# Performance work log

Measured on AMD Instinct MI355X. Metric: run time of the kernel, lower is better.

## Reference

```python
import jax, jax.numpy as jnp
import numpy as np

DIM = 1024
S_SIZE = 512
M_SIZE = 4096
L_SIZE = 8192
MERGE_THRESHOLD = 0.98
L_ALPHA = 0.1
K_PROMOTE = max(1, S_SIZE // 4)  # torch: min(len(candidates), max(1, s_size//4)); candidates >> s_size here


def _l2norm(x, axis=-1):
    # F.normalize(p=2) with eps clamp
    return x / jnp.maximum(jnp.linalg.norm(x, axis=axis, keepdims=True), 1e-12)


def _update(processed_tokens, s_memory, m_memory, l_memory, m_utility, l_utility, wq, bq, wk, bk, s_ptr):
    cand = processed_tokens.reshape(-1, DIM)
    # --- S tier: scatter top-k-norm candidates into ring buffer (vectorized; K<=S so slots distinct) ---
    norms = jnp.linalg.norm(cand, axis=1)
    _, top_idx = jax.lax.top_k(norms, K_PROMOTE)
    pos = (s_ptr + jnp.arange(K_PROMOTE)) % S_SIZE
    s_mem = s_memory.at[pos].set(cand[top_idx])
    s_ptr_new = (s_ptr + K_PROMOTE) % S_SIZE
    # --- promotion attention (1 head, only attn weights used): pick best short-term slot ---
    q = l_memory.mean(axis=0) @ wq.T + bq                      # [dim]
    kproj = s_mem @ wk.T + bk                                  # [S, dim]
    attn = jax.nn.softmax(kproj @ q / jnp.sqrt(jnp.asarray(DIM, cand.dtype)))
    best_s_idx = jnp.argmax(attn)
    candidate = s_mem[best_s_idx]                              # [dim]

    # --- M tier: promote / merge / replace ---
    def not_full(mm, mu):
        ridx = jnp.argmin(mu)
        return mm.at[ridx].set(candidate), mu.at[ridx].set(mu.mean() + 1e-5)

    def full(mm, mu):
        mm_norm = _l2norm(mm)
        sims = mm_norm @ _l2norm(candidate)                    # [M]
        msi = jnp.argmax(sims)
        sim_cand = sims[msi]

        def merge_with_candidate(mm, mu):
            merged = _l2norm((mm[msi] + candidate) / 2.0)
            return mm.at[msi].set(merged), mu.at[msi].set((mu[msi] + mu.mean()) / 2.0)

        def try_internal_merge(mm, mu):
            # most redundant pair: strict lower triangle of cosine sim matrix
            sim_mat = mm_norm @ mm_norm.T                      # [M, M]
            sim_mat = jnp.where(jnp.triu(jnp.ones((M_SIZE, M_SIZE), bool)), -1.0, sim_mat)
            flat = jnp.argmax(sim_mat)
            internal_sim = sim_mat.reshape(-1)[flat]
            idx1, idx2 = flat // M_SIZE, flat % M_SIZE

            def do_pair_merge(mm, mu):
                merged = _l2norm((mm[idx1] + mm[idx2]) / 2.0)
                mm2 = mm.at[idx1].set(merged).at[idx2].set(candidate)
                mu1 = mu.at[idx1].set((mu[idx1] + mu[idx2]) / 2.0)
                mu2 = mu1.at[idx2].set(mu1.mean() + 1e-5)      # torch recomputes mean after idx1 write
                return mm2, mu2

            def replace_weakest(mm, mu):
                li = jnp.argmin(mu)
                stronger = jnp.linalg.norm(candidate) > jnp.linalg.norm(mm[li])
                mm2 = jnp.where(stronger, mm.at[li].set(candidate), mm)
                mu2 = jnp.where(stronger, mu.at[li].set(mu.mean() + 1e-5), mu)
                return mm2, mu2

            return jax.lax.cond(internal_sim > MERGE_THRESHOLD, do_pair_merge, replace_weakest, mm, mu)

        return jax.lax.cond(sim_cand > MERGE_THRESHOLD, merge_with_candidate, try_internal_merge, mm, mu)

    is_m_full = ~jnp.any(m_utility == 0)
    m_mem, m_util = jax.lax.cond(is_m_full, full, not_full, m_memory, m_utility)
    # --- L tier: consolidate most-used M slot into least-used L slot ---
    mi = jnp.argmax(m_util)
    lj = jnp.argmin(l_utility)
    consolidated = (1.0 - L_ALPHA) * l_memory[lj] + L_ALPHA * m_mem[mi]
    l_mem = l_memory.at[lj].set(consolidated)
    l_util = l_utility.at[lj].set(l_utility.mean())            # mean of pre-write values
    return s_mem, m_mem, l_mem, m_util, l_util, s_ptr_new


def setup_inputs() -> dict:
    key = jax.random.key(0)
    ks = jax.random.split(key, 10)
    scale = 1.0 / np.sqrt(DIM)
    return {
        "processed_tokens": jax.random.normal(ks[0], (4, 4096, DIM), jnp.float32),
        "s_memory": jax.random.normal(ks[1], (S_SIZE, DIM), jnp.float32),
        "m_memory": jax.random.normal(ks[2], (M_SIZE, DIM), jnp.float32),
        "l_memory": jax.random.normal(ks[3], (L_SIZE, DIM), jnp.float32),
        "m_utility": jax.random.uniform(ks[4], (M_SIZE,), jnp.float32) + 0.01,  # >0 -> 'm full' branch
        "l_utility": jax.random.uniform(ks[5], (L_SIZE,), jnp.float32) + 0.01,
        "wq": jax.random.normal(ks[6], (DIM, DIM), jnp.float32) * scale,
        "bq": jnp.zeros((DIM,), jnp.float32),
        "wk": jax.random.normal(ks[7], (DIM, DIM), jnp.float32) * scale,
        "bk": jnp.zeros((DIM,), jnp.float32),
        "s_ptr": 0,
    }


def reference(processed_tokens, s_memory, m_memory, l_memory, m_utility, l_utility, wq, bq, wk, bk, s_ptr):
    return _update(processed_tokens, s_memory, m_memory, l_memory, m_utility, l_utility, wq, bq, wk, bk, s_ptr)
```

## Files before the change

kernel.cpp:

```cpp
#include <hip/hip_runtime.h>

#define DIMV 1024
#define SSZ 512
#define MSZ 4096
#define LSZ 8192
#define KPROM 128
#define NCAND 16384
#define NPAIR 528

typedef __attribute__((ext_vector_type(4))) float f32x4;
typedef __attribute__((ext_vector_type(4))) unsigned int u32x4;
typedef __attribute__((ext_vector_type(4))) unsigned short u16x4;
typedef __attribute__((ext_vector_type(8))) __bf16 bf16x8;

#define OUT_S 0ull
#define OUT_M 524288ull
#define OUT_L 4718592ull
#define OUT_MU 13107200ull
#define OUT_LU 13111296ull
#define OUT_SPTR 13119488ull

#define SC_BF16 0ull
#define SC_NORMS 2100000ull
#define SC_TOPIDX 2117000ull
#define SC_LPART 2120000ull
#define SC_RV 2260000ull
#define SC_LMEAN 2262000ull
#define SC_BPK 2414000ull
#define SC_MNORM 2415000ull
#define SC_SIMS 2420000ull
#define SC_PPV 2425000ull
#define SC_PPI 2427000ull

__device__ __forceinline__ float wave_sum(float v) {
#pragma unroll
  for (int o = 32; o > 0; o >>= 1) v += __shfl_down(v, o, 64);
  return v;
}
__device__ __forceinline__ void wave_maxidx(float& v, int& i) {
#pragma unroll
  for (int o = 32; o > 0; o >>= 1) {
    float ov = __shfl_down(v, o, 64);
    int oi = __shfl_down(i, o, 64);
    if (ov > v || (ov == v && oi < i)) { v = ov; i = oi; }
  }
}
__device__ __forceinline__ void wave_minidx(float& v, int& i) {
#pragma unroll
  for (int o = 32; o > 0; o >>= 1) {
    float ov = __shfl_down(v, o, 64);
    int oi = __shfl_down(i, o, 64);
    if (ov < v || (ov == v && oi < i)) { v = ov; i = oi; }
  }
}
__device__ __forceinline__ unsigned short f2bf(float x) {
  unsigned u = __float_as_uint(x);
  return (unsigned short)((u + 0x7FFFu + ((u >> 16) & 1u)) >> 16);
}
__device__ __forceinline__ void gload16(const unsigned short* g, unsigned short* l) {
  __builtin_amdgcn_global_load_lds((const __attribute__((address_space(1))) unsigned int*)(g),
                                   (__attribute__((address_space(3))) unsigned int*)(l), 16, 0, 0);
}

__global__ void kA(const float* __restrict__ cand, const float* __restrict__ l_memory,
                   const float* __restrict__ m, float* __restrict__ norms,
                   float* __restrict__ lpart, unsigned short* __restrict__ mb,
                   float* __restrict__ mnorm, float* __restrict__ rv,
                   unsigned long long* __restrict__ bestPack) {
  int b = blockIdx.x, t = threadIdx.x, lane = t & 63, w = t >> 6;
  if (b < 128) {
    if (b == 0) {
      f32x4 z = {0.f, 0.f, 0.f, 0.f};
      ((f32x4*)rv)[t] = z;
      if (t == 0) bestPack[0] = 0ull;
    }
    f32x4 a0 = {0.f, 0.f, 0.f, 0.f}, a1 = a0, a2 = a0, a3 = a0;
    const f32x4* base = (const f32x4*)(l_memory + (size_t)b * 64 * DIMV);
#pragma unroll 4
    for (int r = 0; r < 64; r += 4) {
      a0 += base[(r + 0) * 256 + t];
      a1 += base[(r + 1) * 256 + t];
      a2 += base[(r + 2) * 256 + t];
      a3 += base[(r + 3) * 256 + t];
    }
    f32x4 a = (a0 + a1) + (a2 + a3);
    ((f32x4*)(lpart + (size_t)b * DIMV))[t] = a;
  } else if (b < 1152) {
    int r0 = (b - 128) * 16 + w * 4;
    const f32x4* base4 = (const f32x4*)(cand + (size_t)r0 * DIMV);
    float s0 = 0.f, s1 = 0.f, s2 = 0.f, s3 = 0.f;
#pragma unroll
    for (int k = 0; k < 16; ++k) {
      f32x4 v = base4[k * 64 + lane];
      float d = v.x * v.x + v.y * v.y + v.z * v.z + v.w * v.w;
      if (k < 4) s0 += d;
      else if (k < 8) s1 += d;
      else if (k < 12) s2 += d;
      else s3 += d;
    }
    f32x4 sv = {s0, s1, s2, s3};
#pragma unroll
    for (int o = 32; o > 0; o >>= 1) {
      sv.x += __shfl_down(sv.x, o, 64);
      sv.y += __shfl_down(sv.y, o, 64);
      sv.z += __shfl_down(sv.z, o, 64);
      sv.w += __shfl_down(sv.w, o, 64);
    }
    if (lane == 0) {
      f32x4 o4 = {sqrtf(sv.x), sqrtf(sv.y), sqrtf(sv.z), sqrtf(sv.w)};
      *((f32x4*)(norms + r0)) = o4;
    }
  } else {
    int r0 = (b - 1152) * 16 + w * 4;
    const f32x4* base4 = (const f32x4*)(m + (size_t)r0 * DIMV);
    u16x4* mb4 = (u16x4*)(mb + (size_t)r0 * DIMV);
    float s0 = 0.f, s1 = 0.f, s2 = 0.f, s3 = 0.f;
#pragma unroll
    for (int k = 0; k < 16; ++k) {
      int i = k * 64 + lane;
      f32x4 v = base4[i];
      float d = v.x * v.x + v.y * v.y + v.z * v.z + v.w * v.w;
      if (k < 4) s0 += d;
      else if (k < 8) s1 += d;
      else if (k < 12) s2 += d;
      else s3 += d;
      u16x4 h;
      h.x = f2bf(v.x); h.y = f2bf(v.y); h.z = f2bf(v.z); h.w = f2bf(v.w);
      mb4[i] = h;
    }
    f32x4 sv = {s0, s1, s2, s3};
#pragma unroll
    for (int o = 32; o > 0; o >>= 1) {
      sv.x += __shfl_down(sv.x, o, 64);
      sv.y += __shfl_down(sv.y, o, 64);
      sv.z += __shfl_down(sv.z, o, 64);
      sv.w += __shfl_down(sv.w, o, 64);
    }
    if (lane == 0) {
      f32x4 o4 = {sqrtf(sv.x), sqrtf(sv.y), sqrtf(sv.z), sqrtf(sv.w)};
      *((f32x4*)(mnorm + r0)) = o4;
    }
  }
}

__device__ int scan_excl_1024(int v, int* sh, int* total) {
  int t = threadIdx.x;
  sh[t] = v;
  __syncthreads();
  for (int o = 1; o < 1024; o <<= 1) {
    int x = (t >= o) ? sh[t - o] : 0;
    __syncthreads();
    sh[t] += x;
    __syncthreads();
  }
  int incl = sh[t];
  *total = sh[1023];
  __syncthreads();
  return incl - v;
}

__global__ void kT(const float* __restrict__ norms, int* __restrict__ topidx,
                   const float* __restrict__ lpart, float* __restrict__ lmean) {
  int t = threadIdx.x;
  if (blockIdx.x == 1) {
    float s0 = 0.f, s1 = 0.f, s2 = 0.f, s3 = 0.f;
    for (int p = 0; p < 128; p += 4) {
      s0 += lpart[(size_t)(p + 0) * DIMV + t];
      s1 += lpart[(size_t)(p + 1) * DIMV + t];
      s2 += lpart[(size_t)(p + 2) * DIMV + t];
      s3 += lpart[(size_t)(p + 3) * DIMV + t];
    }
    lmean[t] = ((s0 + s1) + (s2 + s3)) * (1.f / 8192.f);
    return;
  }
  int w = t >> 6;
  __shared__ int sh[1024];
  __shared__ int histW[16][257];
  __shared__ unsigned s_selkey[KPROM];
  __shared__ int s_selidx[KPROM];
  __shared__ int s_digit, s_sub;
  unsigned key[16];
#pragma unroll
  for (int j = 0; j < 16; ++j) key[j] = __float_as_uint(norms[t * 16 + j]);

  unsigned prefix = 0, himask = 0;
  int remaining = KPROM;
  for (int p = 24; p >= 0; p -= 8) {
    for (int i = t; i < 16 * 257; i += 1024) ((int*)histW)[i] = 0;
    __syncthreads();
#pragma unroll
    for (int j = 0; j < 16; ++j)
      if ((key[j] & himask) == prefix) atomicAdd(&histW[w][(key[j] >> p) & 255], 1);
    __syncthreads();
    if (t < 256) {
      int h = 0;
#pragma unroll
      for (int w2 = 0; w2 < 16; ++w2) h += histW[w2][t];
      sh[t] = h;
    }
    __syncthreads();
    for (int o = 1; o < 256; o <<= 1) {
      int x = (t < 256 && t + o < 256) ? sh[t + o] : 0;
      __syncthreads();
      if (t < 256) sh[t] += x;
      __syncthreads();
    }
    if (t < 256) {
      int sfex = (t < 255) ? sh[t + 1] : 0;
      if (sfex < remaining && remaining <= sh[t]) { s_digit = t; s_sub = sfex; }
    }
    __syncthreads();
    prefix |= ((unsigned)s_digit) << p;
    remaining -= s_sub;
    himask |= (0xFFu << p);
    __syncthreads();
  }
  unsigned T = prefix;

  int cgt = 0, ceq = 0;
#pragma unroll
  for (int j = 0; j < 16; ++j) { cgt += (key[j] > T); ceq += (key[j] == T); }
  int total_pk;
  int spk = scan_excl_1024((cgt << 15) | ceq, sh, &total_pk);
  int sgt = spk >> 15, seq = spk & 0x7FFF;
  int total_gt = total_pk >> 15;
  int need_eq = KPROM - total_gt;
  int g = sgt, e = seq;
#pragma unroll
  for (int j = 0; j < 16; ++j) {
    if (key[j] > T) { s_selkey[g] = key[j]; s_selidx[g] = t * 16 + j; ++g; }
    else if (key[j] == T) {
      if (e < need_eq) { s_selkey[total_gt + e] = key[j]; s_selidx[total_gt + e] = t * 16 + j; }
      ++e;
    }
  }
  __syncthreads();
  if (t < KPROM) {
    unsigned mk = s_selkey[t];
    int mi = s_selidx[t];
    int rank = 0;
    for (int q2 = 0; q2 < KPROM; ++q2) {
      unsigned qk = s_selkey[q2];
      int qi = s_selidx[q2];
      rank += (qk > mk || (qk == mk && qi < mi)) ? 1 : 0;
    }
    topidx[rank] = mi;
  }
}

__global__ void kBC(const float* __restrict__ cand, const float* __restrict__ s_memory,
                    const int* __restrict__ topidx, const int* __restrict__ s_ptr,
                    const float* __restrict__ wq, const float* __restrict__ bq,
                    const float* __restrict__ wk, const float* __restrict__ lmean,
                    float* __restrict__ out_s, float* __restrict__ out_sptr,
                    float* __restrict__ rv) {
  int b = blockIdx.x, t = threadIdx.x, lane = t & 63, w = t >> 6;
  if (b < 512) {
    int sp = s_ptr[0];
    int k = (b - sp + SSZ) & (SSZ - 1);
    const float* src = (k < KPROM) ? (cand + (size_t)topidx[k] * DIMV) : (s_memory + (size_t)b * DIMV);
    ((f32x4*)(out_s + (size_t)b * DIMV))[t] = ((const f32x4*)src)[t];
    if (b == 0 && t == 0) out_sptr[0] = (float)((sp + KPROM) % SSZ);
    return;
  }
  __shared__ float qs[8];
  int qb = b - 512;
  const f32x4* lm = (const f32x4*)lmean;
#pragma unroll
  for (int rr = 0; rr < 2; ++rr) {
    int d = qb * 8 + w * 2 + rr;
    const f32x4* row = (const f32x4*)(wq + (size_t)d * DIMV);
    float s = 0.f;
#pragma unroll
    for (int c = 0; c < 4; ++c) {
      f32x4 a = row[c * 64 + lane], bb = lm[c * 64 + lane];
      s += a.x * bb.x + a.y * bb.y + a.z * bb.z + a.w * bb.w;
    }
    s = wave_sum(s);
    if (lane == 0) qs[w * 2 + rr] = s + bq[d];
  }
  __syncthreads();
  f32x4 a = {0.f, 0.f, 0.f, 0.f};
#pragma unroll
  for (int r = 0; r < 8; ++r) {
    float qd = qs[r];
    f32x4 v = ((const f32x4*)(wk + (size_t)(qb * 8 + r) * DIMV))[t];
    a += v * qd;
  }
  atomicAdd(&rv[t * 4 + 0], a.x);
  atomicAdd(&rv[t * 4 + 1], a.y);
  atomicAdd(&rv[t * 4 + 2], a.z);
  atomicAdd(&rv[t * 4 + 3], a.w);
}

__global__ void kD(const float* __restrict__ out_s, const float* __restrict__ rv,
                   unsigned long long* __restrict__ bestPack) {
  __shared__ unsigned long long spk[4];
  int t = threadIdx.x, lane = t & 63, w = t >> 6;
  int srow = blockIdx.x * 4 + w;
  const f32x4* a = (const f32x4*)(out_s + (size_t)srow * DIMV);
  const f32x4* b = (const f32x4*)rv;
  float s = 0.f;
#pragma unroll
  for (int c = 0; c < 4; ++c) {
    f32x4 x = a[c * 64 + lane], y = b[c * 64 + lane];
    s += x.x * y.x + x.y * y.y + x.z * y.z + x.w * y.w;
  }
  s = wave_sum(s);
  if (lane == 0) {
    unsigned u = __float_as_uint(s);
    u = (u & 0x80000000u) ? ~u : (u | 0x80000000u);
    spk[w] = ((unsigned long long)u << 32) | (unsigned)(~srow);
  }
  __syncthreads();
  if (t == 0) {
    unsigned long long m0 = spk[0];
    for (int i = 1; i < 4; ++i)
      if (spk[i] > m0) m0 = spk[i];
    atomicMax(bestPack, m0);
  }
}

__global__ __launch_bounds__(256, 3) void kG(const unsigned short* __restrict__ mb,
                                             const float* __restrict__ mnorm,
                                             const float* __restrict__ m,
                                             const float* __restrict__ out_s,
                                             const unsigned long long* __restrict__ bestPack,
                                             float* __restrict__ pv, int* __restrict__ pidx,
                                             float* __restrict__ sims) {
  int b = blockIdx.x, t = threadIdx.x, lane = t & 63, w = t >> 6;
  if (b >= NPAIR) {
    int row = (b - NPAIR) * 4 + w;
    int bi = ~((unsigned)(bestPack[0] & 0xFFFFFFFFull));
    const f32x4* mp = (const f32x4*)(m + (size_t)row * DIMV);
    const f32x4* cp = (const f32x4*)(out_s + (size_t)bi * DIMV);
    float sd = 0.f, cd = 0.f;
#pragma unroll
    for (int c = 0; c < 4; ++c) {
      int i = c * 64 + lane;
      f32x4 v = mp[i], u = cp[i];
      sd += v.x * u.x + v.y * u.y + v.z * u.z + v.w * u.w;
      cd += u.x * u.x + u.y * u.y + u.z * u.z + u.w * u.w;
    }
    sd = wave_sum(sd);
    cd = wave_sum(cd);
    if (lane == 0)
      sims[row] = sd / (fmaxf(mnorm[row], 1e-12f) * fmaxf(sqrtf(cd), 1e-12f));
    return;
  }
  __shared__ unsigned short Ash[128 * 64];
  __shared__ unsigned short Bsh[128 * 64];
  __shared__ float spv[4];
  __shared__ int spi[4];

  int bs = (b & 7) * 66 + (b >> 3);
  int bi = (int)((sqrtf(8.f * (float)bs + 1.f) - 1.f) * 0.5f);
  while (bi * (bi + 1) / 2 > bs) --bi;
  while ((bi + 1) * (bi + 2) / 2 <= bs) ++bi;
  int bj = bs - bi * (bi + 1) / 2;
  int rowA0 = bi * 128, rowB0 = bj * 128;

  int wr = w >> 1, wc = w & 1;
  int rl = lane & 15, kq4 = lane >> 4;
  int swz = rl & 7;
  int subrow = lane >> 3, gg = lane & 7;
  int gsw = (gg ^ subrow) << 3;

  f32x4 acc[4][4];
  f32x4 z = {0.f, 0.f, 0.f, 0.f};
#pragma unroll
  for (int ti = 0; ti < 4; ++ti)
#pragma unroll
    for (int tj = 0; tj < 4; ++tj) acc[ti][tj] = z;

  for (int kc = 0; kc < DIMV; kc += 64) {
#pragma unroll
    for (int jj = 0; jj < 4; ++jj) {
      int rsub = w * 32 + jj * 8 + subrow;
      gload16(mb + (size_t)(rowA0 + rsub) * DIMV + kc + gsw, Ash + (w * 4 + jj) * 512);
      gload16(mb + (size_t)(rowB0 + rsub) * DIMV + kc + gsw, Bsh + (w * 4 + jj) * 512);
    }
    __syncthreads();
#pragma unroll
    for (int ks = 0; ks < 2; ++ks) {
      int co = (((ks * 4 + kq4) ^ swz) << 3);
      bf16x8 af[4], bfv[4];
#pragma unroll
      for (int ti = 0; ti < 4; ++ti)
        af[ti] = *(const bf16x8*)(Ash + (wr * 64 + ti * 16 + rl) * 64 + co);
#pragma unroll
      for (int tj = 0; tj < 4; ++tj)
        bfv[tj] = *(const bf16x8*)(Bsh + (wc * 64 + tj * 16 + rl) * 64 + co);
#pragma unroll
      for (int ti = 0; ti < 4; ++ti)
#pragma unroll
        for (int tj = 0; tj < 4; ++tj)
          acc[ti][tj] = __builtin_amdgcn_mfma_f32_16x16x32_bf16(af[ti], bfv[tj], acc[ti][tj], 0, 0, 0);
    }
    __syncthreads();
  }

  float ni[16], nj4[4];
#pragma unroll
  for (int ti = 0; ti < 4; ++ti)
#pragma unroll
    for (int r = 0; r < 4; ++r)
      ni[ti * 4 + r] = fmaxf(mnorm[rowA0 + wr * 64 + ti * 16 + kq4 * 4 + r], 1e-12f);
#pragma unroll
  for (int tj = 0; tj < 4; ++tj)
    nj4[tj] = fmaxf(mnorm[rowB0 + wc * 64 + tj * 16 + rl], 1e-12f);

  float bv = -3.402823466e38f;
  int bidx = 0x7FFFFFFF;
#pragma unroll
  for (int ti = 0; ti < 4; ++ti)
#pragma unroll
    for (int tj = 0; tj < 4; ++tj)
#pragma unroll
      for (int r = 0; r < 4; ++r) {
        int gi = rowA0 + wr * 64 + ti * 16 + kq4 * 4 + r;
        int gj = rowB0 + wc * 64 + tj * 16 + rl;
        if (gi > gj) {
          float s = acc[ti][tj][r] / (ni[ti * 4 + r] * nj4[tj]);
          int fi = gi * MSZ + gj;
          if (s > bv || (s == bv && fi < bidx)) { bv = s; bidx = fi; }
        }
      }
  wave_maxidx(bv, bidx);
  if (lane == 0) { spv[w] = bv; spi[w] = bidx; }
  __syncthreads();
  if (t == 0) {
    float a = spv[0]; int ai = spi[0];
    for (int i = 1; i < 4; ++i)
      if (spv[i] > a || (spv[i] == a && spi[i] < ai)) { a = spv[i]; ai = spi[i]; }
    pv[b] = a;
    pidx[b] = ai;
  }
}

__global__ void kH(const float* __restrict__ pv, const int* __restrict__ pidx,
                   const float* __restrict__ sims, const float* __restrict__ mu,
                   const float* __restrict__ mnorm,
                   const unsigned long long* __restrict__ bestPack,
                   const float* __restrict__ lu, const float* __restrict__ out_s,
                   float* __restrict__ out_mu, float* __restrict__ out_lu,
                   int* __restrict__ ws) {
  __shared__ float swv[16];
  __shared__ int swi[16];
  __shared__ float ssum[16];
  __shared__ int szf[16];
  __shared__ float s_res[2];
  __shared__ int s_resi[2];
  __shared__ int s_branch, s_i1, s_i2, s_lj, s_bi;
  __shared__ float s_u1, s_u2, s_lmean, s_cn;
  int t = threadIdx.x, lane = t & 63, w = t >> 6;

  if (t == 0) s_bi = ~((unsigned)(bestPack[0] & 0xFFFFFFFFull));
  __syncthreads();
  {
    float cs = 0.f;
    if (t < 256) {
      f32x4 c4 = ((const f32x4*)(out_s + (size_t)s_bi * DIMV))[t];
      cs = c4.x * c4.x + c4.y * c4.y + c4.z * c4.z + c4.w * c4.w;
    }
    cs = wave_sum(cs);
    if (lane == 0) ssum[w] = cs;
    __syncthreads();
    if (t == 0) {
      float s2 = 0.f;
      for (int i = 0; i < 16; ++i) s2 += ssum[i];
      s_cn = sqrtf(s2);
    }
    __syncthreads();
  }

  float bv = -3.402823466e38f;
  int bidx = 0x7FFFFFFF;
  for (int i = t; i < NPAIR; i += 1024) {
    float v = pv[i];
    int fi = pidx[i];
    if (v > bv || (v == bv && fi < bidx)) { bv = v; bidx = fi; }
  }
  wave_maxidx(bv, bidx);
  if (lane == 0) { swv[w] = bv; swi[w] = bidx; }
  __syncthreads();
  if (t == 0) {
    float a = swv[0]; int ai = swi[0];
    for (int i = 1; i < 16; ++i)
      if (swv[i] > a || (swv[i] == a && swi[i] < ai)) { a = swv[i]; ai = swi[i]; }
    s_res[0] = a; s_resi[0] = ai;
  }
  __syncthreads();

  bv = -3.402823466e38f;
  bidx = 0x7FFFFFFF;
#pragma unroll
  for (int j = 0; j < 4; ++j) {
    int i = t * 4 + j;
    float v = sims[i];
    if (v > bv) { bv = v; bidx = i; }
  }
  wave_maxidx(bv, bidx);
  if (lane == 0) { swv[w] = bv; swi[w] = bidx; }
  __syncthreads();
  if (t == 0) {
    float a = swv[0]; int ai = swi[0];
    for (int i = 1; i < 16; ++i)
      if (swv[i] > a || (swv[i] == a && swi[i] < ai)) { a = swv[i]; ai = swi[i]; }
    s_res[1] = a; s_resi[1] = ai;
  }
  __syncthreads();

  float muv[4];
  float sum = 0.f, mnv = 3.402823466e38f;
  int mni = 0x7FFFFFFF, zf = 0;
#pragma unroll
  for (int j = 0; j < 4; ++j) {
    int i = t * 4 + j;
    float v = mu[i];
    muv[j] = v;
    sum += v;
    if (v < mnv) { mnv = v; mni = i; }
    if (v == 0.f) zf = 1;
  }
  sum = wave_sum(sum);
  wave_minidx(mnv, mni);
#pragma unroll
  for (int o = 32; o > 0; o >>= 1) zf |= __shfl_down(zf, o, 64);
  if (lane == 0) { ssum[w] = sum; swv[w] = mnv; swi[w] = mni; szf[w] = zf; }
  __syncthreads();
  if (t == 0) {
    float muSum = 0.f;
    int anyz = 0;
    float a = swv[0]; int li = swi[0];
    for (int i = 0; i < 16; ++i) {
      muSum += ssum[i];
      anyz |= szf[i];
      if (i > 0 && (swv[i] < a || (swv[i] == a && swi[i] < li))) { a = swv[i]; li = swi[i]; }
    }
    float muMean = muSum / 4096.f;
    float internal_sim = s_res[0];
    int iflat = s_resi[0];
    float sim_cand = s_res[1];
    int msi = s_resi[1];
    int branch, i1 = -1, i2 = -1;
    float u1 = 0.f, u2 = 0.f;
    if (anyz) {
      branch = 0; i1 = li; u1 = muMean + 1e-5f;
    } else if (sim_cand > 0.98f) {
      branch = 1; i1 = msi; u1 = (mu[msi] + muMean) * 0.5f;
    } else if (internal_sim > 0.98f) {
      branch = 2; i1 = iflat / MSZ; i2 = iflat - (iflat / MSZ) * MSZ;
      float o1 = mu[i1], o2 = mu[i2];
      u1 = (o1 + o2) * 0.5f;
      u2 = (muSum - o1 + u1) / 4096.f + 1e-5f;
    } else {
      if (s_cn > mnorm[li]) { branch = 0; i1 = li; u1 = muMean + 1e-5f; }
      else branch = 4;
    }
    s_branch = branch; s_i1 = i1; s_i2 = i2; s_u1 = u1; s_u2 = u2;
    ws[2] = branch; ws[3] = i1; ws[4] = i2; ws[5] = s_bi;
  }
  __syncthreads();

  int branch = s_branch, i1 = s_i1, i2 = s_i2;
  float u1 = s_u1, u2 = s_u2;
  bv = -3.402823466e38f;
  bidx = 0x7FFFFFFF;
#pragma unroll
  for (int j = 0; j < 4; ++j) {
    int i = t * 4 + j;
    float v = muv[j];
    if (branch != 4 && i == i1) v = u1;
    if (branch == 2 && i == i2) v = u2;
    out_mu[i] = v;
    if (v > bv) { bv = v; bidx = i; }
  }
  wave_maxidx(bv, bidx);
  __syncthreads();
  if (lane == 0) { swv[w] = bv; swi[w] = bidx; }
  __syncthreads();
  if (t == 0) {
    float a = swv[0]; int ai = swi[0];
    for (int i = 1; i < 16; ++i)
      if (swv[i] > a || (swv[i] == a && swi[i] < ai)) { a = swv[i]; ai = swi[i]; }
    ws[1] = ai;
  }

  float luv[8];
  sum = 0.f; mnv = 3.402823466e38f; mni = 0x7FFFFFFF;
#pragma unroll
  for (int j = 0; j < 8; ++j) {
    int i = t * 8 + j;
    float v = lu[i];
    luv[j] = v;
    sum += v;
    if (v < mnv) { mnv = v; mni = i; }
  }
  sum = wave_sum(sum);
  wave_minidx(mnv, mni);
  __syncthreads();
  if (lane == 0) { swv[w] = mnv; swi[w] = mni; ssum[w] = sum; }
  __syncthreads();
  if (t == 0) {
    float a = swv[0]; int ai = swi[0];
    float ls = 0.f;
    for (int i = 0; i < 16; ++i) {
      ls += ssum[i];
      if (i > 0 && (swv[i] < a || (swv[i] == a && swi[i] < ai))) { a = swv[i]; ai = swi[i]; }
    }
    s_lj = ai;
    s_lmean = ls / 8192.f;
    ws[0] = ai;
  }
  __syncthreads();
  int lj = s_lj;
  float lmv = s_lmean;
#pragma unroll
  for (int j = 0; j < 8; ++j) {
    int i = t * 8 + j;
    out_lu[i] = (i == lj) ? lmv : luv[j];
  }
}

__global__ void kI(const float* __restrict__ m, const float* __restrict__ l_memory,
                   const float* __restrict__ out_s, const int* __restrict__ ws,
                   float* __restrict__ out_m, float* __restrict__ out_l) {
  __shared__ float sred[4];
  int b = blockIdx.x, t = threadIdx.x, lane = t & 63, w = t >> 6;
  int lj = ws[0], mi = ws[1], branch = ws[2], i1 = ws[3], i2 = ws[4], best = ws[5];
  if (b < 1024) {
    int r0 = b * 4;
    bool special = (branch != 4) &&
                   ((i1 >= r0 && i1 < r0 + 4) || (branch == 2 && i2 >= r0 && i2 < r0 + 4));
    if (!special) {
      const f32x4* src = (const f32x4*)(m + (size_t)r0 * DIMV);
      f32x4* dst = (f32x4*)(out_m + (size_t)r0 * DIMV);
#pragma unroll
      for (int k = 0; k < 4; ++k) dst[k * 256 + t] = src[k * 256 + t];
      return;
    }
    for (int rr = 0; rr < 4; ++rr) {
      int row = r0 + rr;
      int mode = 0;
      if ((branch == 0 && row == i1) || (branch == 2 && row == i2)) mode = 1;
      else if (branch == 1 && row == i1) mode = 2;
      else if (branch == 2 && row == i1) mode = 3;
      f32x4* dst = (f32x4*)(out_m + (size_t)row * DIMV);
      if (mode == 0) {
        dst[t] = ((const f32x4*)(m + (size_t)row * DIMV))[t];
      } else if (mode == 1) {
        dst[t] = ((const f32x4*)(out_s + (size_t)best * DIMV))[t];
      } else {
        f32x4 a = ((const f32x4*)(m + (size_t)row * DIMV))[t];
        f32x4 bb = (mode == 2) ? ((const f32x4*)(out_s + (size_t)best * DIMV))[t]
                               : ((const f32x4*)(m + (size_t)i2 * DIMV))[t];
        f32x4 v = (a + bb) * 0.5f;
        float ss = v.x * v.x + v.y * v.y + v.z * v.z + v.w * v.w;
        ss = wave_sum(ss);
        if (lane == 0) sred[w] = ss;
        __syncthreads();
        float nrm = fmaxf(sqrtf(sred[0] + sred[1] + sred[2] + sred[3]), 1e-12f);
        __syncthreads();
        dst[t] = v / nrm;
      }
    }
  } else {
    int r0 = (b - 1024) * 4;
    bool special = (lj >= r0 && lj < r0 + 4);
    if (!special) {
      const f32x4* src = (const f32x4*)(l_memory + (size_t)r0 * DIMV);
      f32x4* dst = (f32x4*)(out_l + (size_t)r0 * DIMV);
#pragma unroll
      for (int k = 0; k < 4; ++k) dst[k * 256 + t] = src[k * 256 + t];
      return;
    }
    for (int rr = 0; rr < 4; ++rr) {
      int row = r0 + rr;
      f32x4 v = ((const f32x4*)(l_memory + (size_t)row * DIMV))[t];
      if (row == lj) {
        int mode = 0;
        if ((branch == 0 && mi == i1) || (branch == 2 && mi == i2)) mode = 1;
        else if (branch == 1 && mi == i1) mode = 2;
        else if (branch == 2 && mi == i1) mode = 3;
        f32x4 mv;
        if (mode == 0) {
          mv = ((const f32x4*)(m + (size_t)mi * DIMV))[t];
        } else if (mode == 1) {
          mv = ((const f32x4*)(out_s + (size_t)best * DIMV))[t];
        } else {
          f32x4 a = ((const f32x4*)(m + (size_t)mi * DIMV))[t];
          f32x4 bb = (mode == 2) ? ((const f32x4*)(out_s + (size_t)best * DIMV))[t]
                                 : ((const f32x4*)(m + (size_t)i2 * DIMV))[t];
          f32x4 vm = (a + bb) * 0.5f;
          float ss = vm.x * vm.x + vm.y * vm.y + vm.z * vm.z + vm.w * vm.w;
          ss = wave_sum(ss);
          if (lane == 0) sred[w] = ss;
          __syncthreads();
          float nrm = fmaxf(sqrtf(sred[0] + sred[1] + sred[2] + sred[3]), 1e-12f);
          __syncthreads();
          mv = vm / nrm;
        }
        v = v * 0.9f + mv * 0.1f;
      }
      ((f32x4*)(out_l + (size_t)row * DIMV))[t] = v;
    }
  }
}

extern "C" void kernel_launch(void* const* d_in, const int* in_sizes, int n_in,
                              void* d_out, int out_size, void* d_ws, size_t ws_size,
                              hipStream_t stream) {
  const float* cand = (const float*)d_in[0];
  const float* s_memory = (const float*)d_in[1];
  const float* m_memory = (const float*)d_in[2];
  const float* l_memory = (const float*)d_in[3];
  const float* m_utility = (const float*)d_in[4];
  const float* l_utility = (const float*)d_in[5];
  const float* wq = (const float*)d_in[6];
  const float* bq = (const float*)d_in[7];
  const float* wk = (const float*)d_in[8];
  const float* bk = (const float*)d_in[9];
  const int* s_ptr = (const int*)d_in[10];
  (void)bk;

  float* out = (float*)d_out;
  float* out_s = out + OUT_S;
  float* out_m = out + OUT_M;
  float* out_l = out + OUT_L;
  float* out_mu = out + OUT_MU;
  float* out_lu = out + OUT_LU;
  float* out_sptr = out + OUT_SPTR;

  float* lsc = out_l;
  unsigned short* mb = (unsigned short*)(lsc + SC_BF16);
  float* norms = lsc + SC_NORMS;
  int* topidx = (int*)(lsc + SC_TOPIDX);
  float* lpart = lsc + SC_LPART;
  float* rv = lsc + SC_RV;
  float* lmean = lsc + SC_LMEAN;
  unsigned long long* bestPack = (unsigned long long*)(lsc + SC_BPK);
  float* mnorm = lsc + SC_MNORM;
  float* sims = lsc + SC_SIMS;
  float* pv = lsc + SC_PPV;
  int* pidx = (int*)(lsc + SC_PPI);
  int* wsctl = (int*)d_ws;

  kA<<<1408, 256, 0, stream>>>(cand, l_memory, m_memory, norms, lpart, mb, mnorm, rv, bestPack);
  kT<<<2, 1024, 0, stream>>>(norms, topidx, lpart, lmean);
  kBC<<<640, 256, 0, stream>>>(cand, s_memory, topidx, s_ptr, wq, bq, wk, lmean, out_s, out_sptr,
                               rv);
  kD<<<128, 256, 0, stream>>>(out_s, rv, bestPack);
  kG<<<NPAIR + 1024, 256, 0, stream>>>(mb, mnorm, m_memory, out_s, bestPack, pv, pidx, sims);
  kH<<<1, 1024, 0, stream>>>(pv, pidx, sims, m_utility, mnorm, bestPack, l_utility, out_s,
                             out_mu, out_lu, wsctl);
  kI<<<3072, 256, 0, stream>>>(m_memory, l_memory, out_s, wsctl, out_m, out_l);
}
```

Before: 279.4 us.

## Fuse pairwise M-similarity GEMM into top-k launch to overlap with selection

Moves the candidate-independent all-pairs M-similarity bf16 MFMA tiles out of the later kG kernel and into the launch that does the radix top-k and L-mean. The tiles now run as extra blocks alongside the single-block serial top-k. The remaining kGs kernel only computes the candidate-to-M similarities. Because of the shared 1024-thread block shape, three quarters of each GEMM block's threads exit at once. The 1024-thread launch bound also limits registers for the MFMA accumulators, which risks spills and lower occupancy for that GEMM.

```diff
diff --git a/kernel.cpp b/kernel.cpp
--- a/kernel.cpp
+++ b/kernel.cpp
@@ -159,10 +159,18 @@
   return incl - v;
 }
 
-__global__ void kT(const float* __restrict__ norms, int* __restrict__ topidx,
-                   const float* __restrict__ lpart, float* __restrict__ lmean) {
-  int t = threadIdx.x;
-  if (blockIdx.x == 1) {
+__global__ __launch_bounds__(1024) void kTG(
+    const float* __restrict__ norms, int* __restrict__ topidx,
+    const float* __restrict__ lpart, float* __restrict__ lmean,
+    const unsigned short* __restrict__ mb, const float* __restrict__ mnorm,
+    float* __restrict__ pv, int* __restrict__ pidx) {
+  __shared__ __align__(16) char smem[33024];
+  __shared__ int s_digit, s_sub;
+  __shared__ float spv[4];
+  __shared__ int spi[4];
+  int b = blockIdx.x, t = threadIdx.x;
+
+  if (b == 1) {
     float s0 = 0.f, s1 = 0.f, s2 = 0.f, s3 = 0.f;
     for (int p = 0; p < 128; p += 4) {
       s0 += lpart[(size_t)(p + 0) * DIMV + t];
@@ -173,12 +181,105 @@
     lmean[t] = ((s0 + s1) + (s2 + s3)) * (1.f / 8192.f);
     return;
   }
+
+  if (b >= 2) {
+    if (t >= 256) return;
+    unsigned short* Ash = (unsigned short*)smem;
+    unsigned short* Bsh = (unsigned short*)(smem + 16384);
+    int lane = t & 63, w = t >> 6;
+    int tb = b - 2;
+    int bs = (tb & 7) * 66 + (tb >> 3);
+    int bi = (int)((sqrtf(8.f * (float)bs + 1.f) - 1.f) * 0.5f);
+    while (bi * (bi + 1) / 2 > bs) --bi;
+    while ((bi + 1) * (bi + 2) / 2 <= bs) ++bi;
+    int bj = bs - bi * (bi + 1) / 2;
+    int rowA0 = bi * 128, rowB0 = bj * 128;
+
+    int wr = w >> 1, wc = w & 1;
+    int rl = lane & 15, kq4 = lane >> 4;
+    int swz = rl & 7;
+    int subrow = lane >> 3, gg = lane & 7;
+    int gsw = (gg ^ subrow) << 3;
+
+    f32x4 acc[4][4];
+    f32x4 z = {0.f, 0.f, 0.f, 0.f};
+#pragma unroll
+    for (int ti = 0; ti < 4; ++ti)
+#pragma unroll
+      for (int tj = 0; tj < 4; ++tj) acc[ti][tj] = z;
+
+    for (int kc = 0; kc < DIMV; kc += 64) {
+#pragma unroll
+      for (int jj = 0; jj < 4; ++jj) {
+        int rsub = w * 32 + jj * 8 + subrow;
+        gload16(mb + (size_t)(rowA0 + rsub) * DIMV + kc + gsw, Ash + (w * 4 + jj) * 512);
+        gload16(mb + (size_t)(rowB0 + rsub) * DIMV + kc + gsw, Bsh + (w * 4 + jj) * 512);
+      }
+      __syncthreads();
+#pragma unroll
+      for (int ks = 0; ks < 2; ++ks) {
+        int co = (((ks * 4 + kq4) ^ swz) << 3);
+        bf16x8 af[4], bfv[4];
+#pragma unroll
+        for (int ti = 0; ti < 4; ++ti)
+          af[ti] = *(const bf16x8*)(Ash + (wr * 64 + ti * 16 + rl) * 64 + co);
+#pragma unroll
+        for (int tj = 0; tj < 4; ++tj)
+          bfv[tj] = *(const bf16x8*)(Bsh + (wc * 64 + tj * 16 + rl) * 64 + co);
+#pragma unroll
+        for (int ti = 0; ti < 4; ++ti)
+#pragma unroll
+          for (int tj = 0; tj < 4; ++tj)
+            acc[ti][tj] =
+                __builtin_amdgcn_mfma_f32_16x16x32_bf16(af[ti], bfv[tj], acc[ti][tj], 0, 0, 0);
+      }
+      __syncthreads();
+    }
+
+    float ni[16], nj4[4];
+#pragma unroll
+    for (int ti = 0; ti < 4; ++ti)
+#pragma unroll
+      for (int r = 0; r < 4; ++r)
+        ni[ti * 4 + r] = fmaxf(mnorm[rowA0 + wr * 64 + ti * 16 + kq4 * 4 + r], 1e-12f);
+#pragma unroll
+    for (int tj = 0; tj < 4; ++tj)
+      nj4[tj] = fmaxf(mnorm[rowB0 + wc * 64 + tj * 16 + rl], 1e-12f);
+
+    float bv = -3.402823466e38f;
+    int bidx = 0x7FFFFFFF;
+#pragma unroll
+    for (int ti = 0; ti < 4; ++ti)
+#pragma unroll
+      for (int tj = 0; tj < 4; ++tj)
+#pragma unroll
+        for (int r = 0; r < 4; ++r) {
+          int gi = rowA0 + wr * 64 + ti * 16 + kq4 * 4 + r;
+          int gj = rowB0 + wc * 64 + tj * 16 + rl;
+          if (gi > gj) {
+            float s = acc[ti][tj][r] / (ni[ti * 4 + r] * nj4[tj]);
+            int fi = gi * MSZ + gj;
+            if (s > bv || (s == bv && fi < bidx)) { bv = s; bidx = fi; }
+          }
+        }
+    wave_maxidx(bv, bidx);
+    if (lane == 0) { spv[w] = bv; spi[w] = bidx; }
+    __syncthreads();
+    if (t == 0) {
+      float a = spv[0]; int ai = spi[0];
+      for (int i = 1; i < 4; ++i)
+        if (spv[i] > a || (spv[i] == a && spi[i] < ai)) { a = spv[i]; ai = spi[i]; }
+      pv[tb] = a;
+      pidx[tb] = ai;
+    }
+    return;
+  }
+
+  int* sh = (int*)smem;
+  int* histW = (int*)(smem + 4096);
+  unsigned* s_selkey = (unsigned*)(smem + 4096 + 16448);
+  int* s_selidx = (int*)(smem + 4096 + 16448 + 512);
   int w = t >> 6;
-  __shared__ int sh[1024];
-  __shared__ int histW[16][257];
-  __shared__ unsigned s_selkey[KPROM];
-  __shared__ int s_selidx[KPROM];
-  __shared__ int s_digit, s_sub;
   unsigned key[16];
 #pragma unroll
   for (int j = 0; j < 16; ++j) key[j] = __float_as_uint(norms[t * 16 + j]);
@@ -186,16 +287,16 @@
   unsigned prefix = 0, himask = 0;
   int remaining = KPROM;
   for (int p = 24; p >= 0; p -= 8) {
-    for (int i = t; i < 16 * 257; i += 1024) ((int*)histW)[i] = 0;
+    for (int i = t; i < 16 * 257; i += 1024) histW[i] = 0;
     __syncthreads();
 #pragma unroll
     for (int j = 0; j < 16; ++j)
-      if ((key[j] & himask) == prefix) atomicAdd(&histW[w][(key[j] >> p) & 255], 1);
+      if ((key[j] & himask) == prefix) atomicAdd(&histW[w * 257 + ((key[j] >> p) & 255)], 1);
     __syncthreads();
     if (t < 256) {
       int h = 0;
 #pragma unroll
-      for (int w2 = 0; w2 < 16; ++w2) h += histW[w2][t];
+      for (int w2 = 0; w2 < 16; ++w2) h += histW[w2 * 257 + t];
       sh[t] = h;
     }
     __syncthreads();
@@ -321,121 +422,27 @@
   }
 }
 
-__global__ __launch_bounds__(256, 3) void kG(const unsigned short* __restrict__ mb,
-                                             const float* __restrict__ mnorm,
-                                             const float* __restrict__ m,
-                                             const float* __restrict__ out_s,
-                                             const unsigned long long* __restrict__ bestPack,
-                                             float* __restrict__ pv, int* __restrict__ pidx,
-                                             float* __restrict__ sims) {
+__global__ void kGs(const float* __restrict__ mnorm, const float* __restrict__ m,
+                    const float* __restrict__ out_s,
+                    const unsigned long long* __restrict__ bestPack,
+                    float* __restrict__ sims) {
   int b = blockIdx.x, t = threadIdx.x, lane = t & 63, w = t >> 6;
-  if (b >= NPAIR) {
-    int row = (b - NPAIR) * 4 + w;
-    int bi = ~((unsigned)(bestPack[0] & 0xFFFFFFFFull));
-    const f32x4* mp = (const f32x4*)(m + (size_t)row * DIMV);
-    const f32x4* cp = (const f32x4*)(out_s + (size_t)bi * DIMV);
-    float sd = 0.f, cd = 0.f;
-#pragma unroll
-    for (int c = 0; c < 4; ++c) {
-      int i = c * 64 + lane;
-      f32x4 v = mp[i], u = cp[i];
-      sd += v.x * u.x + v.y * u.y + v.z * u.z + v.w * u.w;
-      cd += u.x * u.x + u.y * u.y + u.z * u.z + u.w * u.w;
-    }
-    sd = wave_sum(sd);
-    cd = wave_sum(cd);
-    if (lane == 0)
-      sims[row] = sd / (fmaxf(mnorm[row], 1e-12f) * fmaxf(sqrtf(cd), 1e-12f));
-    return;
-  }
-  __shared__ unsigned short Ash[128 * 64];
-  __shared__ unsigned short Bsh[128 * 64];
-  __shared__ float spv[4];
-  __shared__ int spi[4];
-
-  int bs = (b & 7) * 66 + (b >> 3);
-  int bi = (int)((sqrtf(8.f * (float)bs + 1.f) - 1.f) * 0.5f);
-  while (bi * (bi + 1) / 2 > bs) --bi;
-  while ((bi + 1) * (bi + 2) / 2 <= bs) ++bi;
-  int bj = bs - bi * (bi + 1) / 2;
-  int rowA0 = bi * 128, rowB0 = bj * 128;
-
-  int wr = w >> 1, wc = w & 1;
-  int rl = lane & 15, kq4 = lane >> 4;
-  int swz = rl & 7;
-  int subrow = lane >> 3, gg = lane & 7;
-  int gsw = (gg ^ subrow) << 3;
-
-  f32x4 acc[4][4];
-  f32x4 z = {0.f, 0.f, 0.f, 0.f};
-#pragma unroll
-  for (int ti = 0; ti < 4; ++ti)
-#pragma unroll
-    for (int tj = 0; tj < 4; ++tj) acc[ti][tj] = z;
-
-  for (int kc = 0; kc < DIMV; kc += 64) {
-#pragma unroll
-    for (int jj = 0; jj < 4; ++jj) {
-      int rsub = w * 32 + jj * 8 + subrow;
-      gload16(mb + (size_t)(rowA0 + rsub) * DIMV + kc + gsw, Ash + (w * 4 + jj) * 512);
-      gload16(mb + (size_t)(rowB0 + rsub) * DIMV + kc + gsw, Bsh + (w * 4 + jj) * 512);
-    }
-    __syncthreads();
-#pragma unroll
-    for (int ks = 0; ks < 2; ++ks) {
-      int co = (((ks * 4 + kq4) ^ swz) << 3);
-      bf16x8 af[4], bfv[4];
-#pragma unroll
-      for (int ti = 0; ti < 4; ++ti)
-        af[ti] = *(const bf16x8*)(Ash + (wr * 64 + ti * 16 + rl) * 64 + co);
-#pragma unroll
-      for (int tj = 0; tj < 4; ++tj)
-        bfv[tj] = *(const bf16x8*)(Bsh + (wc * 64 + tj * 16 + rl) * 64 + co);
-#pragma unroll
-      for (int ti = 0; ti < 4; ++ti)
-#pragma unroll
-        for (int tj = 0; tj < 4; ++tj)
-          acc[ti][tj] = __builtin_amdgcn_mfma_f32_16x16x32_bf16(af[ti], bfv[tj], acc[ti][tj], 0, 0, 0);
-    }
-    __syncthreads();
-  }
-
-  float ni[16], nj4[4];
-#pragma unroll
-  for (int ti = 0; ti < 4; ++ti)
-#pragma unroll
-    for (int r = 0; r < 4; ++r)
-      ni[ti * 4 + r] = fmaxf(mnorm[rowA0 + wr * 64 + ti * 16 + kq4 * 4 + r], 1e-12f);
-#pragma unroll
-  for (int tj = 0; tj < 4; ++tj)
-    nj4[tj] = fmaxf(mnorm[rowB0 + wc * 64 + tj * 16 + rl], 1e-12f);
-
-  float bv = -3.402823466e38f;
-  int bidx = 0x7FFFFFFF;
-#pragma unroll
-  for (int ti = 0; ti < 4; ++ti)
-#pragma unroll
-    for (int tj = 0; tj < 4; ++tj)
-#pragma unroll
-      for (int r = 0; r < 4; ++r) {
-        int gi = rowA0 + wr * 64 + ti * 16 + kq4 * 4 + r;
-        int gj = rowB0 + wc * 64 + tj * 16 + rl;
-        if (gi > gj) {
-          float s = acc[ti][tj][r] / (ni[ti * 4 + r] * nj4[tj]);
-          int fi = gi * MSZ + gj;
-          if (s > bv || (s == bv && fi < bidx)) { bv = s; bidx = fi; }
-        }
-      }
-  wave_maxidx(bv, bidx);
-  if (lane == 0) { spv[w] = bv; spi[w] = bidx; }
-  __syncthreads();
-  if (t == 0) {
-    float a = spv[0]; int ai = spi[0];
-    for (int i = 1; i < 4; ++i)
-      if (spv[i] > a || (spv[i] == a && spi[i] < ai)) { a = spv[i]; ai = spi[i]; }
-    pv[b] = a;
-    pidx[b] = ai;
-  }
+  int row = b * 4 + w;
+  int bi = ~((unsigned)(bestPack[0] & 0xFFFFFFFFull));
+  const f32x4* mp = (const f32x4*)(m + (size_t)row * DIMV);
+  const f32x4* cp = (const f32x4*)(out_s + (size_t)bi * DIMV);
+  float sd = 0.f, cd = 0.f;
+#pragma unroll
+  for (int c = 0; c < 4; ++c) {
+    int i = c * 64 + lane;
+    f32x4 v = mp[i], u = cp[i];
+    sd += v.x * u.x + v.y * u.y + v.z * u.z + v.w * u.w;
+    cd += u.x * u.x + u.y * u.y + u.z * u.z + u.w * u.w;
+  }
+  sd = wave_sum(sd);
+  cd = wave_sum(cd);
+  if (lane == 0)
+    sims[row] = sd / (fmaxf(mnorm[row], 1e-12f) * fmaxf(sqrtf(cd), 1e-12f));
 }
 
 __global__ void kH(const float* __restrict__ pv, const int* __restrict__ pidx,
@@ -747,11 +754,11 @@
   int* wsctl = (int*)d_ws;
 
   kA<<<1408, 256, 0, stream>>>(cand, l_memory, m_memory, norms, lpart, mb, mnorm, rv, bestPack);
-  kT<<<2, 1024, 0, stream>>>(norms, topidx, lpart, lmean);
+  kTG<<<NPAIR + 2, 1024, 0, stream>>>(norms, topidx, lpart, lmean, mb, mnorm, pv, pidx);
   kBC<<<640, 256, 0, stream>>>(cand, s_memory, topidx, s_ptr, wq, bq, wk, lmean, out_s, out_sptr,
                                rv);
   kD<<<128, 256, 0, stream>>>(out_s, rv, bestPack);
-  kG<<<NPAIR + 1024, 256, 0, stream>>>(mb, mnorm, m_memory, out_s, bestPack, pv, pidx, sims);
+  kGs<<<1024, 256, 0, stream>>>(mnorm, m_memory, out_s, bestPack, sims);
   kH<<<1, 1024, 0, stream>>>(pv, pidx, sims, m_utility, mnorm, bestPack, l_utility, out_s,
                              out_mu, out_lu, wsctl);
   kI<<<3072, 256, 0, stream>>>(m_memory, l_memory, out_s, wsctl, out_m, out_l);
```

Result: slower. 294.1 us (+5.3%).
